# Kernel tuning notes

Hardware: AMD Instinct MI355X
Metric: run time of the kernel (lower is better)

The kernel has to match this reference:

```python
import jax, jax.numpy as jnp
import numpy as np

# ViT-Small config
L, D, H, HD = 12, 384, 6, 64
P, IMG, NCLS = 16, 224, 1000
NPATCH = (IMG // P) ** 2  # 196
GAMMA, MIN_TOKENS, EPS = 0.5, 16, 1e-6
SCALE = HD ** -0.5


def _ln(x, w, b, eps=1e-6):
    mu = jnp.mean(x, axis=-1, keepdims=True)
    var = jnp.var(x, axis=-1, keepdims=True)
    return (x - mu) * jax.lax.rsqrt(var + eps) * w + b


def _qkv_split(xn, w, b):
    # xn: [B, Nt, D] -> q,k,v each [B, H, Nt, HD]
    B, Nt, _ = xn.shape
    qkv = (xn @ w.T + b).reshape(B, Nt, 3, H, HD).transpose(2, 0, 3, 1, 4)
    return qkv[0], qkv[1], qkv[2]


def _vit_forward(x, patch_w, patch_b, cls_token, pos_embed,
                 ln1_w, ln1_b, qkv_w, qkv_b, proj_w, proj_b,
                 ln2_w, ln2_b, fc1_w, fc1_b, fc2_w, fc2_b,
                 norm_w, norm_b, head_w, head_b, keep_schedule=None):
    B = x.shape[0]
    # patch embed: conv stride 16 -> [B, D, 14, 14] -> [B, 196, D]
    xp = jax.lax.conv_general_dilated(x, patch_w, (P, P), 'VALID',
                                      dimension_numbers=('NCHW', 'OIHW', 'NCHW'))
    xp = xp.reshape(B, D, NPATCH).transpose(0, 2, 1) + patch_b
    cls = jnp.broadcast_to(cls_token, (B, 1, D))
    xt = jnp.concatenate([cls, xp], axis=1) + pos_embed  # [B, 197, D]

    N = NPATCH
    prev_mass = jnp.asarray(1.0, jnp.float32)
    schedule = []
    for l in range(L):
        if keep_schedule is not None:
            keep_idx = keep_schedule[l]
        elif N > MIN_TOKENS:
            # CLS-only attention importance scoring (cheap pass)
            xn = _ln(xt, ln1_w[l], ln1_b[l])
            q, k, v = _qkv_split(xn, qkv_w[l], qkv_b[l])
            a_cls = jax.nn.softmax(jnp.einsum('bhqd,bhkd->bhqk', q[:, :, :1], k) * SCALE, axis=-1)[:, :, 0, :]  # [B,H,Nt]
            vnorm = jnp.linalg.norm(v, axis=-1)  # [B,H,Nt]
            imp = (a_cls * vnorm).mean(axis=1)   # [B,Nt]
            imp_p = imp[:, 1:]                   # patch importance
            mass = jnp.mean(imp_p.sum(-1) / (imp.sum(-1) + EPS))
            keep_ratio = float(jnp.clip(GAMMA * mass / (prev_mass + EPS), 0.0, 1.0))
            N_next = max(MIN_TOKENS, int(N * keep_ratio))
            if N_next < N:
                scores = imp_p.mean(0)  # shared keep set across batch (index_select semantics)
                top = jax.lax.top_k(scores, N_next)[1]
                keep_idx = jnp.concatenate([jnp.zeros((1,), jnp.int32),
                                            jnp.sort(top).astype(jnp.int32) + 1])
            else:
                keep_idx = None
            prev_mass = mass
        else:
            keep_idx = None
        schedule.append(keep_idx)
        if keep_idx is not None:
            xt = jnp.take(xt, keep_idx, axis=1)
            N = int(keep_idx.shape[0]) - 1

        # full transformer block on surviving tokens
        Nt = xt.shape[1]
        xn = _ln(xt, ln1_w[l], ln1_b[l])
        q, k, v = _qkv_split(xn, qkv_w[l], qkv_b[l])
        a = jax.nn.softmax(jnp.einsum('bhqd,bhkd->bhqk', q, k) * SCALE, axis=-1)
        o = jnp.einsum('bhqk,bhkd->bhqd', a, v).transpose(0, 2, 1, 3).reshape(B, Nt, D)
        xt = xt + o @ proj_w[l].T + proj_b[l]
        h = _ln(xt, ln2_w[l], ln2_b[l])
        h = jax.nn.gelu(h @ fc1_w[l].T + fc1_b[l], approximate=False)
        xt = xt + h @ fc2_w[l].T + fc2_b[l]

    xt = _ln(xt, norm_w, norm_b)
    logits = xt[:, 0] @ head_w.T + head_b
    return logits, schedule


def setup_inputs() -> dict:
    key = jax.random.key(0)
    ks = jax.random.split(key, 10)
    rn = lambda k, s, sc=0.02: jax.random.normal(k, s, jnp.float32) * sc
    return {
        'x': jax.random.normal(ks[0], (64, 3, IMG, IMG), jnp.float32),
        'patch_w': rn(ks[1], (D, 3, P, P)),
        'patch_b': jnp.zeros((D,), jnp.float32),
        'cls_token': rn(ks[2], (1, 1, D)),
        'pos_embed': rn(ks[3], (1, NPATCH + 1, D)),
        'ln1_w': jnp.ones((L, D), jnp.float32), 'ln1_b': jnp.zeros((L, D), jnp.float32),
        'qkv_w': rn(ks[4], (L, 3 * D, D)), 'qkv_b': jnp.zeros((L, 3 * D), jnp.float32),
        'proj_w': rn(ks[5], (L, D, D)), 'proj_b': jnp.zeros((L, D), jnp.float32),
        'ln2_w': jnp.ones((L, D), jnp.float32), 'ln2_b': jnp.zeros((L, D), jnp.float32),
        'fc1_w': rn(ks[6], (L, 4 * D, D)), 'fc1_b': jnp.zeros((L, 4 * D), jnp.float32),
        'fc2_w': rn(ks[7], (L, D, 4 * D)), 'fc2_b': jnp.zeros((L, D), jnp.float32),
        'norm_w': jnp.ones((D,), jnp.float32), 'norm_b': jnp.zeros((D,), jnp.float32),
        'head_w': rn(ks[8], (NCLS, D)), 'head_b': jnp.zeros((NCLS,), jnp.float32),
    }


def reference(x, patch_w, patch_b, cls_token, pos_embed, ln1_w, ln1_b, qkv_w, qkv_b,
              proj_w, proj_b, ln2_w, ln2_b, fc1_w, fc1_b, fc2_w, fc2_b,
              norm_w, norm_b, head_w, head_b):
    logits, _ = _vit_forward(x, patch_w, patch_b, cls_token, pos_embed, ln1_w, ln1_b,
                             qkv_w, qkv_b, proj_w, proj_b, ln2_w, ln2_b,
                             fc1_w, fc1_b, fc2_w, fc2_b, norm_w, norm_b, head_w, head_b)
    return logits
```

## Files before the change

kernel.cpp:

```cpp
#include <hip/hip_runtime.h>
#include <hip/hip_bf16.h>

static constexpr int kL = 12;
static constexpr int kD = 384;
static constexpr int kH = 6;
static constexpr int kB = 64;
static constexpr int kNP = 196;
static constexpr int kBAND = 197;
static constexpr int kNCLS = 1000;
static constexpr float kSCALE = 0.125f;
static constexpr float kEPS = 1e-6f;
static constexpr size_t kWQ = (size_t)kB * kH * kBAND * 64;

typedef __attribute__((ext_vector_type(8))) short short8;
typedef __attribute__((ext_vector_type(4))) float f32x4;

__device__ __forceinline__ float gelu_f(float x) {
    return 0.5f * x * (1.0f + erff(x * 0.70710678118654752440f));
}
__device__ __forceinline__ unsigned short f2bf(float x) {
    __hip_bfloat16 h = __float2bfloat16(x);
    return *(unsigned short*)&h;
}
__device__ __forceinline__ float bf2f(unsigned short u) {
    __hip_bfloat16 h = *(__hip_bfloat16*)&u;
    return __bfloat162float(h);
}

__global__ __launch_bounds__(384) void k_init(int* si, float* sf,
                                              const float* __restrict__ cls,
                                              const float* __restrict__ pos,
                                              float* __restrict__ xtA,
                                              float2* __restrict__ pstats) {
    int b = blockIdx.x, c = threadIdx.x;
    float v = cls[c] + pos[c];
    xtA[(size_t)b * kBAND * kD + c] = v;
    __shared__ float r1[384], r2[384];
    r1[c] = v; r2[c] = v * v;
    __syncthreads();
    if (c < 128) { r1[c] += r1[c + 128] + r1[c + 256]; r2[c] += r2[c + 128] + r2[c + 256]; }
    __syncthreads();
    for (int st = 64; st; st >>= 1) {
        if (c < st) { r1[c] += r1[c + st]; r2[c] += r2[c + st]; }
        __syncthreads();
    }
    if (c == 0) {
        pstats[(size_t)(b * kBAND) * 8 + 0] = make_float2(r1[0], r2[0]);
#pragma unroll
        for (int nn = 1; nn < 6; ++nn) pstats[(size_t)(b * kBAND) * 8 + nn] = make_float2(0.f, 0.f);
        if (b == 0) { si[0] = kBAND; sf[0] = 1.0f; }
    }
}

__global__ __launch_bounds__(256) void k_cvtall(
    const float* __restrict__ s0, const float* __restrict__ s1, const float* __restrict__ s2,
    const float* __restrict__ s3, const float* __restrict__ s4,
    __hip_bfloat16* __restrict__ d0, __hip_bfloat16* __restrict__ d1, __hip_bfloat16* __restrict__ d2,
    __hip_bfloat16* __restrict__ d3, __hip_bfloat16* __restrict__ d4) {
    const int c0 = 73728, c1 = 1400832, c2 = 1843200, c3 = 3612672, c4 = 5382144;
    int stride = gridDim.x * 256;
    for (int i = blockIdx.x * 256 + threadIdx.x; i < c4; i += stride) {
        const float* src; __hip_bfloat16* dst; int off;
        if (i < c0)      { src = s0; dst = d0; off = i; }
        else if (i < c1) { src = s1; dst = d1; off = i - c0; }
        else if (i < c2) { src = s2; dst = d2; off = i - c1; }
        else if (i < c3) { src = s3; dst = d3; off = i - c2; }
        else             { src = s4; dst = d4; off = i - c3; }
        float4 v = ((const float4*)src)[off];
        dst[4 * off + 0] = __float2bfloat16(v.x);
        dst[4 * off + 1] = __float2bfloat16(v.y);
        dst[4 * off + 2] = __float2bfloat16(v.z);
        dst[4 * off + 3] = __float2bfloat16(v.w);
    }
}

__global__ __launch_bounds__(256) void k_im2col(const float* __restrict__ x, __hip_bfloat16* __restrict__ A) {
    int pt = blockIdx.x;
    int b = pt / kNP, t = pt - b * kNP;
    int py = t / 14, px = t - py * 14;
    const float* xb = x + (size_t)b * 3 * 224 * 224;
    __hip_bfloat16* arow = A + (size_t)pt * 768;
    for (int k = threadIdx.x; k < 768; k += 256) {
        int c = k >> 8;
        int r = k & 255;
        int ky = r >> 4, kx = r & 15;
        arow[k] = __float2bfloat16(xb[((size_t)c * 224 + py * 16 + ky) * 224 + px * 16 + kx]);
    }
}

template<int OUT_BF16, int ACT_GELU, int MODE, int LNA, int STATS>
__global__ __launch_bounds__(256) void k_mgemm(
    const void* __restrict__ Av, int lda,
    const unsigned short* __restrict__ W, int K,
    const float* __restrict__ bias,
    void* __restrict__ Cv, int ldc,
    const float* __restrict__ R,
    const int* __restrict__ keepR,
    const float* __restrict__ lnw, const float* __restrict__ lnb,
    int rT, int nT, int band,
    const int* __restrict__ NtPtr, int ntConst,
    const float2* __restrict__ pstatsIn, float2* __restrict__ pstatsOut)
{
    __shared__ __align__(16) unsigned char pool[18432];
    unsigned short (*As)[72] = (unsigned short (*)[72])pool;
    unsigned short (*Ws)[72] = (unsigned short (*)[72])(pool + 9216);
    float (*Cs)[66] = (float (*)[66])pool;
    unsigned short (*Cu)[76] = (unsigned short (*)[76])pool;
    __shared__ float mus[64], rss[64];

    int Nt = NtPtr ? NtPtr[0] : ntConst;
    unsigned int rowsTotal = (unsigned int)kB * (unsigned int)Nt;

    int L = blockIdx.x;
    int xcd = L & 7;
    int m = L >> 3;
    int n = m % nT;
    int r = (m / nT) * 8 + xcd;
    if (r >= rT) return;
    unsigned int r0 = (unsigned int)r * 64;
    int n0 = n * 64;
    if (r0 >= rowsTotal) return;

    int tid = threadIdx.x;
    int srow = tid >> 3;
    int scol = (tid & 7) << 3;

    unsigned int rv0 = r0 + srow, rv1 = r0 + srow + 32;
    bool v0 = rv0 < rowsTotal, v1 = rv1 < rowsTotal;
    const unsigned short* ah0 = nullptr; const unsigned short* ah1 = nullptr;
    const float* af0 = nullptr; const float* af1 = nullptr;
    if (v0) {
        unsigned int bb = rv0 / (unsigned int)Nt, tt = rv0 - bb * Nt;
        size_t prow = (size_t)bb * band + tt;
        if (LNA) af0 = (const float*)Av + prow * lda;
        else     ah0 = (const unsigned short*)Av + prow * lda;
    }
    if (v1) {
        unsigned int bb = rv1 / (unsigned int)Nt, tt = rv1 - bb * Nt;
        size_t prow = (size_t)bb * band + tt;
        if (LNA) af1 = (const float*)Av + prow * lda;
        else     ah1 = (const unsigned short*)Av + prow * lda;
    }
    const unsigned short* wp0 = W + (size_t)(n0 + srow) * K;
    const unsigned short* wp1 = W + (size_t)(n0 + srow + 32) * K;

    float mu0 = 0.f, rs0 = 0.f, mu1 = 0.f, rs1 = 0.f;
    if (LNA) {
        if (tid < 64) {
            unsigned int rv = r0 + tid;
            float mu = 0.f, rsd = 0.f;
            if (rv < rowsTotal) {
                unsigned int bb = rv / (unsigned int)Nt, tt = rv - bb * Nt;
                const float2* ps = pstatsIn + ((size_t)bb * band + tt) * 8;
                float s1 = 0.f, s2 = 0.f;
#pragma unroll
                for (int nn = 0; nn < 6; ++nn) { float2 p = ps[nn]; s1 += p.x; s2 += p.y; }
                mu = s1 * (1.f / 384.f);
                float var = fmaxf(s2 * (1.f / 384.f) - mu * mu, 0.f);
                rsd = rsqrtf(var + kEPS);
            }
            mus[tid] = mu; rss[tid] = rsd;
        }
        __syncthreads();
        mu0 = mus[srow]; rs0 = rss[srow];
        mu1 = mus[srow + 32]; rs1 = rss[srow + 32];
    }

    int wave = tid >> 6, lane = tid & 63;
    int wr32 = ((wave >> 1) & 1) * 32, wc32 = (wave & 1) * 32;
    int l15 = lane & 15, l4 = lane >> 4;

    f32x4 acc00 = {}, acc01 = {}, acc10 = {}, acc11 = {};

    for (int k0 = 0; k0 < K; k0 += 64) {
        uint4 zero = make_uint4(0, 0, 0, 0);
        uint4 a0 = zero, a1 = zero;
        uint4 w0 = *(const uint4*)(wp0 + k0 + scol);
        uint4 w1 = *(const uint4*)(wp1 + k0 + scol);
        if (LNA) {
            float4 lw0 = *(const float4*)(lnw + k0 + scol);
            float4 lw1 = *(const float4*)(lnw + k0 + scol + 4);
            float4 lb0 = *(const float4*)(lnb + k0 + scol);
            float4 lb1 = *(const float4*)(lnb + k0 + scol + 4);
            if (v0) {
                float4 x0 = *(const float4*)(af0 + k0 + scol);
                float4 x1 = *(const float4*)(af0 + k0 + scol + 4);
                unsigned short p[8];
                p[0] = f2bf((x0.x - mu0) * rs0 * lw0.x + lb0.x);
                p[1] = f2bf((x0.y - mu0) * rs0 * lw0.y + lb0.y);
                p[2] = f2bf((x0.z - mu0) * rs0 * lw0.z + lb0.z);
                p[3] = f2bf((x0.w - mu0) * rs0 * lw0.w + lb0.w);
                p[4] = f2bf((x1.x - mu0) * rs0 * lw1.x + lb1.x);
                p[5] = f2bf((x1.y - mu0) * rs0 * lw1.y + lb1.y);
                p[6] = f2bf((x1.z - mu0) * rs0 * lw1.z + lb1.z);
                p[7] = f2bf((x1.w - mu0) * rs0 * lw1.w + lb1.w);
                a0 = *(uint4*)p;
            }
            if (v1) {
                float4 x0 = *(const float4*)(af1 + k0 + scol);
                float4 x1 = *(const float4*)(af1 + k0 + scol + 4);
                unsigned short p[8];
                p[0] = f2bf((x0.x - mu1) * rs1 * lw0.x + lb0.x);
                p[1] = f2bf((x0.y - mu1) * rs1 * lw0.y + lb0.y);
                p[2] = f2bf((x0.z - mu1) * rs1 * lw0.z + lb0.z);
                p[3] = f2bf((x0.w - mu1) * rs1 * lw0.w + lb0.w);
                p[4] = f2bf((x1.x - mu1) * rs1 * lw1.x + lb1.x);
                p[5] = f2bf((x1.y - mu1) * rs1 * lw1.y + lb1.y);
                p[6] = f2bf((x1.z - mu1) * rs1 * lw1.z + lb1.z);
                p[7] = f2bf((x1.w - mu1) * rs1 * lw1.w + lb1.w);
                a1 = *(uint4*)p;
            }
        } else {
            a0 = v0 ? *(const uint4*)(ah0 + k0 + scol) : zero;
            a1 = v1 ? *(const uint4*)(ah1 + k0 + scol) : zero;
        }
        __syncthreads();
        *(uint4*)&As[srow][scol] = a0;
        *(uint4*)&As[srow + 32][scol] = a1;
        *(uint4*)&Ws[srow][scol] = w0;
        *(uint4*)&Ws[srow + 32][scol] = w1;
        __syncthreads();
#pragma unroll
        for (int ks = 0; ks < 2; ++ks) {
            short8 af_0 = *(const short8*)&As[wr32 + l15][ks * 32 + l4 * 8];
            short8 af_1 = *(const short8*)&As[wr32 + 16 + l15][ks * 32 + l4 * 8];
            short8 bf_0 = *(const short8*)&Ws[wc32 + l15][ks * 32 + l4 * 8];
            short8 bf_1 = *(const short8*)&Ws[wc32 + 16 + l15][ks * 32 + l4 * 8];
            acc00 = __builtin_amdgcn_mfma_f32_16x16x32_bf16(af_0, bf_0, acc00, 0, 0, 0);
            acc01 = __builtin_amdgcn_mfma_f32_16x16x32_bf16(af_0, bf_1, acc01, 0, 0, 0);
            acc10 = __builtin_amdgcn_mfma_f32_16x16x32_bf16(af_1, bf_0, acc10, 0, 0, 0);
            acc11 = __builtin_amdgcn_mfma_f32_16x16x32_bf16(af_1, bf_1, acc11, 0, 0, 0);
        }
    }

    __syncthreads();
    f32x4 accs[2][2] = { { acc00, acc01 }, { acc10, acc11 } };
#pragma unroll
    for (int fi = 0; fi < 2; ++fi) {
        int lrow = wr32 + fi * 16 + l4 * 4;
        unsigned int rvb = r0 + lrow;
#pragma unroll
        for (int fj = 0; fj < 2; ++fj) {
            int lcol = wc32 + fj * 16 + l15;
            float bv = bias ? bias[n0 + lcol] : 0.f;
#pragma unroll
            for (int rr = 0; rr < 4; ++rr) {
                unsigned int rv = rvb + rr;
                float v = accs[fi][fj][rr] + bv;
                if (ACT_GELU) v = gelu_f(v);
                if (MODE == 2) {
                    if (rv < rowsTotal) {
                        unsigned int bb = rv / (unsigned int)Nt;
                        unsigned int tt = rv - bb * (unsigned int)Nt;
                        v += R[(size_t)(tt + 1) * kD + n0 + lcol];
                    }
                } else if (R && rv < rowsTotal) {
                    unsigned int bb = rv / (unsigned int)Nt;
                    unsigned int tt = rv - bb * (unsigned int)Nt;
                    size_t rrow = keepR ? ((size_t)bb * band + keepR[tt]) : ((size_t)bb * band + tt);
                    v += R[rrow * ldc + n0 + lcol];
                }
                if (OUT_BF16) Cu[lrow + rr][lcol] = f2bf(v);
                else          Cs[lrow + rr][lcol] = v;
            }
        }
    }
    __syncthreads();

    if (OUT_BF16) {
#pragma unroll
        for (int i = 0; i < 2; ++i) {
            int id = tid + (i << 8);
            int row = id >> 3, c2 = id & 7;
            unsigned int rv = r0 + row;
            if (rv < rowsTotal) {
                unsigned int bb = rv / (unsigned int)Nt;
                unsigned int tt = rv - bb * (unsigned int)Nt;
                uint4 val = *(const uint4*)&Cu[row][c2 << 3];
                if (MODE == 1) {
                    int which = n0 >= 768 ? 2 : (n0 >= 384 ? 1 : 0);
                    int hh = (n0 - which * 384) >> 6;
                    *(uint4*)((__hip_bfloat16*)Cv + (size_t)which * kWQ +
                              (((size_t)bb * kH + hh) * kBAND + tt) * 64 + (c2 << 3)) = val;
                } else {
                    size_t prow = (size_t)bb * band + tt;
                    *(uint4*)((__hip_bfloat16*)Cv + prow * ldc + n0 + (c2 << 3)) = val;
                }
            }
        }
    } else {
#pragma unroll
        for (int i = 0; i < 4; ++i) {
            int id = tid + (i << 8);
            int row = id >> 4, c4 = id & 15;
            unsigned int rv = r0 + row;
            if (rv < rowsTotal) {
                unsigned int bb = rv / (unsigned int)Nt;
                unsigned int tt = rv - bb * (unsigned int)Nt;
                float4 val = *(const float4*)&Cs[row][c4 << 2];
                if (MODE == 2) {
                    *(float4*)((float*)Cv + ((size_t)bb * kBAND + tt + 1) * ldc + n0 + (c4 << 2)) = val;
                } else {
                    *(float4*)((float*)Cv + ((size_t)bb * band + tt) * ldc + n0 + (c4 << 2)) = val;
                }
                if (STATS) {
                    float s1 = (val.x + val.y) + (val.z + val.w);
                    float s2 = (val.x * val.x + val.y * val.y) + (val.z * val.z + val.w * val.w);
#pragma unroll
                    for (int off = 1; off < 16; off <<= 1) {
                        s1 += __shfl_xor(s1, off, 64);
                        s2 += __shfl_xor(s2, off, 64);
                    }
                    if (c4 == 0) {
                        size_t sridx = (MODE == 2) ? ((size_t)bb * kBAND + tt + 1)
                                                   : ((size_t)bb * band + tt);
                        pstatsOut[sridx * 8 + n] = make_float2(s1, s2);
                    }
                }
            }
        }
    }
}

__global__ __launch_bounds__(256) void k_decA(const __hip_bfloat16* __restrict__ qsplit,
                                              float* __restrict__ imph, float* __restrict__ sabh,
                                              const int* __restrict__ si) {
    int Nt = si[0];
    if (Nt - 1 <= 16) return;
    int tid = threadIdx.x, w = tid >> 6, lane = tid & 63;
    int bh = blockIdx.x;
    __shared__ float qs[64];
    __shared__ float sdot[224], svn[224];
    __shared__ float red[256];
    const __hip_bfloat16* qp = qsplit + (size_t)bh * kBAND * 64;
    const __hip_bfloat16* kp = qsplit + kWQ + (size_t)bh * kBAND * 64;
    const __hip_bfloat16* vp = qsplit + 2 * kWQ + (size_t)bh * kBAND * 64;
    if (tid < 64) qs[tid] = __bfloat162float(qp[tid]);
    __syncthreads();
    float qv = qs[lane];
    for (int j = w; j < Nt; j += 8) {
        int j2 = j + 4;
        bool has2 = j2 < Nt;
        float k1 = __bfloat162float(kp[(size_t)j * 64 + lane]);
        float v1 = __bfloat162float(vp[(size_t)j * 64 + lane]);
        float k2 = has2 ? __bfloat162float(kp[(size_t)j2 * 64 + lane]) : 0.f;
        float v2 = has2 ? __bfloat162float(vp[(size_t)j2 * 64 + lane]) : 0.f;
        float p1 = qv * k1, n1 = v1 * v1;
        float p2 = qv * k2, n2 = v2 * v2;
#pragma unroll
        for (int off = 1; off < 64; off <<= 1) {
            p1 += __shfl_xor(p1, off, 64); n1 += __shfl_xor(n1, off, 64);
            p2 += __shfl_xor(p2, off, 64); n2 += __shfl_xor(n2, off, 64);
        }
        if (lane == 0) {
            sdot[j] = p1 * kSCALE; svn[j] = sqrtf(n1);
            if (has2) { sdot[j2] = p2 * kSCALE; svn[j2] = sqrtf(n2); }
        }
    }
    __syncthreads();
    float s = (tid < Nt) ? sdot[tid] : -INFINITY;
    red[tid] = s; __syncthreads();
    for (int st = 128; st; st >>= 1) { if (tid < st) red[tid] = fmaxf(red[tid], red[tid + st]); __syncthreads(); }
    float mmax = red[0]; __syncthreads();
    float e = (tid < Nt) ? expf(s - mmax) : 0.f;
    red[tid] = e; __syncthreads();
    for (int st = 128; st; st >>= 1) { if (tid < st) red[tid] += red[tid + st]; __syncthreads(); }
    float inv = 1.f / red[0];
    float val = (tid < Nt) ? e * inv * svn[tid] : 0.f;
    if (tid < Nt) imph[(size_t)bh * kBAND + tid] = val;
    __syncthreads();
    red[tid] = val; __syncthreads();
    for (int st = 128; st; st >>= 1) { if (tid < st) red[tid] += red[tid + st]; __syncthreads(); }
    if (tid == 0) { sabh[2 * bh] = red[0]; sabh[2 * bh + 1] = val; }
}

__global__ __launch_bounds__(256) void k_decB(int* __restrict__ si, float* __restrict__ sf,
                                              const float* __restrict__ imph,
                                              const float* __restrict__ sabh,
                                              int* __restrict__ keep) {
    int Nt = si[0];
    int tid = threadIdx.x;
    if (Nt - 1 <= 16) {
        for (int j = tid; j < Nt; j += 256) keep[j] = j;
        return;
    }
    int N = Nt - 1;
    __shared__ float red[256];
    float v = 0.f;
    if (tid < kB) {
        float sa = 0.f, i0 = 0.f;
#pragma unroll
        for (int hh = 0; hh < kH; ++hh) {
            sa += sabh[2 * (tid * kH + hh)];
            i0 += sabh[2 * (tid * kH + hh) + 1];
        }
        sa *= (1.f / 6.f); i0 *= (1.f / 6.f);
        v = (sa - i0) / (sa + kEPS);
    }
    red[tid] = v; __syncthreads();
    for (int st = 128; st; st >>= 1) { if (tid < st) red[tid] += red[tid + st]; __syncthreads(); }
    float mass = red[0] * (1.f / 64.f);
    float prev = sf[0];
    float ratio = 0.5f * mass / (prev + kEPS);
    ratio = fminf(fmaxf(ratio, 0.f), 1.f);
    int N_next = (int)((double)N * (double)ratio);
    if (N_next < 16) N_next = 16;
    if (tid == 0) sf[0] = mass;
    __syncthreads();
    if (N_next >= N) {
        for (int j = tid; j < Nt; j += 256) keep[j] = j;
        return;
    }
    __shared__ float sc[200];
    __shared__ int flag[200];
    if (tid < N) {
        float a0 = 0.f, a1 = 0.f, a2 = 0.f, a3 = 0.f;
        const float* p = imph + tid + 1;
#pragma unroll 4
        for (int q = 0; q < kB * kH; q += 4) {
            a0 += p[(size_t)(q + 0) * kBAND];
            a1 += p[(size_t)(q + 1) * kBAND];
            a2 += p[(size_t)(q + 2) * kBAND];
            a3 += p[(size_t)(q + 3) * kBAND];
        }
        sc[tid] = (a0 + a1) + (a2 + a3);
    }
    __syncthreads();
    if (tid < N) {
        float s2 = sc[tid];
        int rank = 0;
        for (int i = 0; i < N; ++i) {
            float o2 = sc[i];
            rank += (o2 > s2) || (o2 == s2 && i < tid);
        }
        flag[tid] = (rank < N_next) ? 1 : 0;
    }
    __syncthreads();
    if (tid == 0) {
        keep[0] = 0;
        int pos = 1;
        for (int j = 0; j < N; ++j) if (flag[j]) keep[pos++] = j + 1;
        si[0] = N_next + 1;
    }
}

__global__ __launch_bounds__(256) void k_attn2(const __hip_bfloat16* __restrict__ qsplit,
                                               __hip_bfloat16* __restrict__ o,
                                               const int* __restrict__ si,
                                               const int* __restrict__ keep) {
    __shared__ __align__(16) unsigned short Kb[224][72];
    __shared__ __align__(16) unsigned short Vt[64][228];
    __shared__ __align__(16) unsigned short Pb[4][16][228];
    int Nt = si[0];
    int bh = blockIdx.x;
    int b = bh / kH, h = bh - b * kH;
    int tid = threadIdx.x, w = tid >> 6, lane = tid & 63;
    int l15 = lane & 15, l4 = lane >> 4;
    int nJT = (Nt + 15) >> 4;
    int nKT = (Nt + 31) >> 5;
    int NTP = nKT << 5;

    const unsigned short* qb = (const unsigned short*)qsplit + (size_t)bh * kBAND * 64;
    const unsigned short* kb = (const unsigned short*)qsplit + kWQ + (size_t)bh * kBAND * 64;
    const unsigned short* vb = (const unsigned short*)qsplit + 2 * kWQ + (size_t)bh * kBAND * 64;

    {
        int rr = tid >> 3;
        int c8 = (tid & 7) << 3;
        for (int r = rr; r < NTP; r += 32) {
            uint4 kv = make_uint4(0, 0, 0, 0), vv = make_uint4(0, 0, 0, 0);
            if (r < Nt) {
                int old = keep[r];
                kv = *(const uint4*)(kb + ((size_t)old << 6) + c8);
                vv = *(const uint4*)(vb + ((size_t)old << 6) + c8);
            }
            *(uint4*)&Kb[r][c8] = kv;
            const unsigned short* vs = (const unsigned short*)&vv;
#pragma unroll
            for (int e = 0; e < 8; ++e) Vt[c8 + e][r] = vs[e];
        }
    }
    __syncthreads();

    for (int strip = w; strip < nJT; strip += 4) {
        int tq = (strip << 4) + l15;
        int told = (tq < Nt) ? keep[tq] : 0;
        const unsigned short* qrow = qb + ((size_t)told << 6) + (l4 << 3);
        short8 qf0 = *(const short8*)(qrow);
        short8 qf1 = *(const short8*)(qrow + 32);

        f32x4 sv[13];
#pragma unroll
        for (int jt = 0; jt < 13; ++jt) {
            if (jt < nJT) {
                const unsigned short* kr = &Kb[(jt << 4) + l15][l4 << 3];
                short8 kf0 = *(const short8*)(kr);
                short8 kf1 = *(const short8*)(kr + 32);
                f32x4 a = {};
                a = __builtin_amdgcn_mfma_f32_16x16x32_bf16(qf0, kf0, a, 0, 0, 0);
                a = __builtin_amdgcn_mfma_f32_16x16x32_bf16(qf1, kf1, a, 0, 0, 0);
                sv[jt] = a;
            }
        }
        float mx[4] = { -INFINITY, -INFINITY, -INFINITY, -INFINITY };
#pragma unroll
        for (int jt = 0; jt < 13; ++jt) if (jt < nJT) {
            bool ok = ((jt << 4) + l15) < Nt;
#pragma unroll
            for (int r = 0; r < 4; ++r) {
                float s = ok ? sv[jt][r] * kSCALE : -INFINITY;
                sv[jt][r] = s;
                mx[r] = fmaxf(mx[r], s);
            }
        }
#pragma unroll
        for (int r = 0; r < 4; ++r) {
            mx[r] = fmaxf(mx[r], __shfl_xor(mx[r], 1, 64));
            mx[r] = fmaxf(mx[r], __shfl_xor(mx[r], 2, 64));
            mx[r] = fmaxf(mx[r], __shfl_xor(mx[r], 4, 64));
            mx[r] = fmaxf(mx[r], __shfl_xor(mx[r], 8, 64));
        }
        float sm[4] = { 0.f, 0.f, 0.f, 0.f };
#pragma unroll
        for (int jt = 0; jt < 13; ++jt) if (jt < nJT) {
#pragma unroll
            for (int r = 0; r < 4; ++r) {
                float p = expf(sv[jt][r] - mx[r]);
                sv[jt][r] = p;
                sm[r] += p;
            }
        }
#pragma unroll
        for (int r = 0; r < 4; ++r) {
            sm[r] += __shfl_xor(sm[r], 1, 64);
            sm[r] += __shfl_xor(sm[r], 2, 64);
            sm[r] += __shfl_xor(sm[r], 4, 64);
            sm[r] += __shfl_xor(sm[r], 8, 64);
            sm[r] = 1.f / sm[r];
        }
#pragma unroll
        for (int jt = 0; jt < 13; ++jt) if (jt < nJT) {
#pragma unroll
            for (int r = 0; r < 4; ++r)
                Pb[w][(l4 << 2) + r][(jt << 4) + l15] = f2bf(sv[jt][r] * sm[r]);
        }
        for (int c = (nJT << 4) + lane; c < NTP; c += 64) {
#pragma unroll
            for (int rr2 = 0; rr2 < 16; ++rr2) Pb[w][rr2][c] = 0;
        }
        asm volatile("s_waitcnt lgkmcnt(0)" ::: "memory");
        __builtin_amdgcn_sched_barrier(0);

        f32x4 oacc[4] = { {}, {}, {}, {} };
#pragma unroll
        for (int kt = 0; kt < 7; ++kt) if (kt < nKT) {
            short8 pf = *(const short8*)&Pb[w][l15][(kt << 5) + (l4 << 3)];
#pragma unroll
            for (int dt = 0; dt < 4; ++dt) {
                short8 vf = *(const short8*)&Vt[(dt << 4) + l15][(kt << 5) + (l4 << 3)];
                oacc[dt] = __builtin_amdgcn_mfma_f32_16x16x32_bf16(pf, vf, oacc[dt], 0, 0, 0);
            }
        }
#pragma unroll
        for (int dt = 0; dt < 4; ++dt) {
#pragma unroll
            for (int r = 0; r < 4; ++r) {
                int tqo = (strip << 4) + (l4 << 2) + r;
                if (tqo < Nt)
                    o[((size_t)b * kBAND + tqo) * kD + h * 64 + (dt << 4) + l15] =
                        __float2bfloat16(oacc[dt][r]);
            }
        }
    }
}

__global__ __launch_bounds__(256) void k_head(const float* __restrict__ X,
                                              const float* __restrict__ nw, const float* __restrict__ nb,
                                              const float* __restrict__ hw, const float* __restrict__ hb,
                                              float* __restrict__ out) {
    int b = blockIdx.x >> 2;
    int tid = threadIdx.x;
    __shared__ float xs[384];
    __shared__ float red[256];
    const float* row = X + (size_t)b * kBAND * kD;
    float s1 = 0.f, s2 = 0.f;
    for (int c = tid; c < 384; c += 256) { float v = row[c]; xs[c] = v; s1 += v; s2 += v * v; }
    red[tid] = s1; __syncthreads();
    for (int st = 128; st; st >>= 1) { if (tid < st) red[tid] += red[tid + st]; __syncthreads(); }
    float sum = red[0]; __syncthreads();
    red[tid] = s2; __syncthreads();
    for (int st = 128; st; st >>= 1) { if (tid < st) red[tid] += red[tid + st]; __syncthreads(); }
    float sq = red[0];
    float mu = sum * (1.f / 384.f);
    float var = fmaxf(sq * (1.f / 384.f) - mu * mu, 0.f);
    float rs = rsqrtf(var + kEPS);
    __syncthreads();
    for (int c = tid; c < 384; c += 256) xs[c] = (xs[c] - mu) * rs * nw[c] + nb[c];
    __syncthreads();
    int n = ((blockIdx.x & 3) << 8) + tid;
    if (n >= kNCLS) return;
    const float* wrow = hw + (size_t)n * kD;
    float acc = 0.f;
#pragma unroll 8
    for (int d = 0; d < kD; d += 4) {
        float4 w4 = *(const float4*)(wrow + d);
        acc += xs[d] * w4.x + xs[d + 1] * w4.y + xs[d + 2] * w4.z + xs[d + 3] * w4.w;
    }
    out[(size_t)b * kNCLS + n] = acc + hb[n];
}

extern "C" void kernel_launch(void* const* d_in, const int* in_sizes, int n_in,
                              void* d_out, int out_size, void* d_ws, size_t ws_size,
                              hipStream_t stream) {
    const float* x       = (const float*)d_in[0];
    const float* patch_w = (const float*)d_in[1];
    const float* patch_b = (const float*)d_in[2];
    const float* cls_tok = (const float*)d_in[3];
    const float* pos     = (const float*)d_in[4];
    const float* ln1w    = (const float*)d_in[5];
    const float* ln1b    = (const float*)d_in[6];
    const float* qkvw    = (const float*)d_in[7];
    const float* qkvb    = (const float*)d_in[8];
    const float* projw   = (const float*)d_in[9];
    const float* projb   = (const float*)d_in[10];
    const float* ln2w    = (const float*)d_in[11];
    const float* ln2b    = (const float*)d_in[12];
    const float* fc1w    = (const float*)d_in[13];
    const float* fc1b    = (const float*)d_in[14];
    const float* fc2w    = (const float*)d_in[15];
    const float* fc2b    = (const float*)d_in[16];
    const float* normw   = (const float*)d_in[17];
    const float* normb   = (const float*)d_in[18];
    const float* headw   = (const float*)d_in[19];
    const float* headb   = (const float*)d_in[20];
    float* out = (float*)d_out;

    char* ws = (char*)d_ws;
    const size_t MB = 1024ull * 1024ull;
    int*   si   = (int*)ws;
    float* sf   = (float*)(ws + 64);
    int*   keep = (int*)(ws + 256);
    float* sabh = (float*)(ws + 4096);
    float* imph = (float*)(ws + 16384);
    float* xtA  = (float*)(ws + 1 * MB);
    float* xtB  = (float*)(ws + 21 * MB);
    __hip_bfloat16* obuf = (__hip_bfloat16*)(ws + 41 * MB);
    __hip_bfloat16* Aim    = (__hip_bfloat16*)(ws + 51 * MB);
    __hip_bfloat16* qsplit = (__hip_bfloat16*)(ws + 51 * MB);
    __hip_bfloat16* hbuf   = (__hip_bfloat16*)(ws + 51 * MB);
    __hip_bfloat16* wpat = (__hip_bfloat16*)(ws + 110 * MB);
    __hip_bfloat16* wqkv = (__hip_bfloat16*)(ws + 111 * MB);
    __hip_bfloat16* wprj = (__hip_bfloat16*)(ws + 122 * MB);
    __hip_bfloat16* wfc1 = (__hip_bfloat16*)(ws + 126 * MB);
    __hip_bfloat16* wfc2 = (__hip_bfloat16*)(ws + 141 * MB);
    float2* pstats = (float2*)(ws + 156 * MB);

    k_init<<<64, 384, 0, stream>>>(si, sf, cls_tok, pos, xtA, pstats);
    k_cvtall<<<2048, 256, 0, stream>>>(patch_w, qkvw, projw, fc1w, fc2w,
                                       wpat, wqkv, wprj, wfc1, wfc2);

    k_im2col<<<kB * kNP, 256, 0, stream>>>(x, Aim);
    k_mgemm<0, 0, 2, 0, 1><<<8 * 6 * 25, 256, 0, stream>>>(
        (const void*)Aim, 768, (const unsigned short*)wpat, 768,
        patch_b, xtA, kD, pos, (const int*)nullptr,
        (const float*)nullptr, (const float*)nullptr,
        196, 6, 196, (const int*)nullptr, 196,
        (const float2*)nullptr, pstats);

    float* cur = xtA; float* oth = xtB;
    for (int l = 0; l < kL; ++l) {
        const float* l1w = ln1w + l * kD;  const float* l1b = ln1b + l * kD;
        const __hip_bfloat16* qw = wqkv + (size_t)l * 1152 * kD;
        const float* qb = qkvb + l * 1152;
        const __hip_bfloat16* pw = wprj + (size_t)l * kD * kD;
        const float* pb = projb + l * kD;
        const float* l2w = ln2w + l * kD;  const float* l2b = ln2b + l * kD;
        const __hip_bfloat16* f1w = wfc1 + (size_t)l * 1536 * kD;
        const float* f1b = fc1b + l * 1536;
        const __hip_bfloat16* f2w = wfc2 + (size_t)l * kD * 1536;
        const float* f2b = fc2b + l * kD;

        k_mgemm<1, 0, 1, 1, 0><<<8 * 18 * 25, 256, 0, stream>>>(
            (const void*)cur, kD, (const unsigned short*)qw, kD,
            qb, qsplit, 1152, (const float*)nullptr, (const int*)nullptr,
            l1w, l1b, 197, 18, kBAND, si, 0,
            (const float2*)pstats, (float2*)nullptr);
        k_decA<<<kB * kH, 256, 0, stream>>>(qsplit, imph, sabh, si);
        k_decB<<<1, 256, 0, stream>>>(si, sf, imph, sabh, keep);
        k_attn2<<<kB * kH, 256, 0, stream>>>(qsplit, obuf, si, keep);
        k_mgemm<0, 0, 0, 0, 1><<<8 * 6 * 25, 256, 0, stream>>>(
            (const void*)obuf, kD, (const unsigned short*)pw, kD,
            pb, oth, kD, cur, keep,
            (const float*)nullptr, (const float*)nullptr,
            197, 6, kBAND, si, 0,
            (const float2*)nullptr, pstats);
        { float* tmp = cur; cur = oth; oth = tmp; }
        k_mgemm<1, 1, 0, 1, 0><<<8 * 24 * 25, 256, 0, stream>>>(
            (const void*)cur, kD, (const unsigned short*)f1w, kD,
            f1b, hbuf, 1536, (const float*)nullptr, (const int*)nullptr,
            l2w, l2b, 197, 24, kBAND, si, 0,
            (const float2*)pstats, (float2*)nullptr);
        k_mgemm<0, 0, 0, 0, 1><<<8 * 6 * 25, 256, 0, stream>>>(
            (const void*)hbuf, 1536, (const unsigned short*)f2w, 1536,
            f2b, cur, kD, cur, (const int*)nullptr,
            (const float*)nullptr, (const float*)nullptr,
            197, 6, kBAND, si, 0,
            (const float2*)nullptr, pstats);
    }

    k_head<<<kB * 4, 256, 0, stream>>>(cur, normw, normb, headw, headb, out);
}
```

Before: 1.251 ms.

## Widen GEMM tiles to 64x128 and transpose importance buffer for coalesced reduction

The generic MFMA GEMM now computes a 64x128 output tile per block: each wave holds 2x4 accumulators, more weight rows are staged in LDS, and fp32 output is written in two 64-column halves. This halves the number of blocks, so each A tile is loaded and LayerNorm-normalized half as often. Per-head stats are written per 64-column half, so the stats layout stays the same. Separately, the importance buffer is stored token-major so the single-block decision kernel can reduce it with coalesced float4 loads across more threads. The larger tile uses more LDS and registers, which lowers occupancy, and with fewer blocks the grid may underfill the GPU for small token counts.

```diff
diff --git a/kernel.cpp b/kernel.cpp
--- a/kernel.cpp
+++ b/kernel.cpp
@@ -11,6 +11,7 @@
 static constexpr float kSCALE = 0.125f;
 static constexpr float kEPS = 1e-6f;
 static constexpr size_t kWQ = (size_t)kB * kH * kBAND * 64;
+static constexpr int kBH = kB * kH;
 
 typedef __attribute__((ext_vector_type(8))) short short8;
 typedef __attribute__((ext_vector_type(4))) float f32x4;
@@ -21,10 +22,6 @@
 __device__ __forceinline__ unsigned short f2bf(float x) {
     __hip_bfloat16 h = __float2bfloat16(x);
     return *(unsigned short*)&h;
-}
-__device__ __forceinline__ float bf2f(unsigned short u) {
-    __hip_bfloat16 h = *(__hip_bfloat16*)&u;
-    return __bfloat162float(h);
 }
 
 __global__ __launch_bounds__(384) void k_init(int* si, float* sf,
@@ -101,11 +98,11 @@
     const int* __restrict__ NtPtr, int ntConst,
     const float2* __restrict__ pstatsIn, float2* __restrict__ pstatsOut)
 {
-    __shared__ __align__(16) unsigned char pool[18432];
+    __shared__ __align__(16) unsigned char pool[27648];
     unsigned short (*As)[72] = (unsigned short (*)[72])pool;
     unsigned short (*Ws)[72] = (unsigned short (*)[72])(pool + 9216);
-    float (*Cs)[66] = (float (*)[66])pool;
-    unsigned short (*Cu)[76] = (unsigned short (*)[76])pool;
+    float (*Cs)[68] = (float (*)[68])pool;
+    unsigned short (*Cu)[136] = (unsigned short (*)[136])pool;
     __shared__ float mus[64], rss[64];
 
     int Nt = NtPtr ? NtPtr[0] : ntConst;
@@ -118,7 +115,7 @@
     int r = (m / nT) * 8 + xcd;
     if (r >= rT) return;
     unsigned int r0 = (unsigned int)r * 64;
-    int n0 = n * 64;
+    int n0 = n * 128;
     if (r0 >= rowsTotal) return;
 
     int tid = threadIdx.x;
@@ -143,6 +140,8 @@
     }
     const unsigned short* wp0 = W + (size_t)(n0 + srow) * K;
     const unsigned short* wp1 = W + (size_t)(n0 + srow + 32) * K;
+    const unsigned short* wp2 = W + (size_t)(n0 + srow + 64) * K;
+    const unsigned short* wp3 = W + (size_t)(n0 + srow + 96) * K;
 
     float mu0 = 0.f, rs0 = 0.f, mu1 = 0.f, rs1 = 0.f;
     if (LNA) {
@@ -167,16 +166,23 @@
     }
 
     int wave = tid >> 6, lane = tid & 63;
-    int wr32 = ((wave >> 1) & 1) * 32, wc32 = (wave & 1) * 32;
+    int wr32 = ((wave >> 1) & 1) << 5;
+    int wc64 = (wave & 1) << 6;
     int l15 = lane & 15, l4 = lane >> 4;
 
-    f32x4 acc00 = {}, acc01 = {}, acc10 = {}, acc11 = {};
+    f32x4 acc[2][4];
+#pragma unroll
+    for (int i = 0; i < 2; ++i)
+#pragma unroll
+        for (int j = 0; j < 4; ++j) acc[i][j] = (f32x4){};
 
     for (int k0 = 0; k0 < K; k0 += 64) {
         uint4 zero = make_uint4(0, 0, 0, 0);
         uint4 a0 = zero, a1 = zero;
         uint4 w0 = *(const uint4*)(wp0 + k0 + scol);
         uint4 w1 = *(const uint4*)(wp1 + k0 + scol);
+        uint4 w2 = *(const uint4*)(wp2 + k0 + scol);
+        uint4 w3 = *(const uint4*)(wp3 + k0 + scol);
         if (LNA) {
             float4 lw0 = *(const float4*)(lnw + k0 + scol);
             float4 lw1 = *(const float4*)(lnw + k0 + scol + 4);
@@ -219,69 +225,59 @@
         *(uint4*)&As[srow + 32][scol] = a1;
         *(uint4*)&Ws[srow][scol] = w0;
         *(uint4*)&Ws[srow + 32][scol] = w1;
+        *(uint4*)&Ws[srow + 64][scol] = w2;
+        *(uint4*)&Ws[srow + 96][scol] = w3;
         __syncthreads();
 #pragma unroll
         for (int ks = 0; ks < 2; ++ks) {
-            short8 af_0 = *(const short8*)&As[wr32 + l15][ks * 32 + l4 * 8];
-            short8 af_1 = *(const short8*)&As[wr32 + 16 + l15][ks * 32 + l4 * 8];
-            short8 bf_0 = *(const short8*)&Ws[wc32 + l15][ks * 32 + l4 * 8];
-            short8 bf_1 = *(const short8*)&Ws[wc32 + 16 + l15][ks * 32 + l4 * 8];
-            acc00 = __builtin_amdgcn_mfma_f32_16x16x32_bf16(af_0, bf_0, acc00, 0, 0, 0);
-            acc01 = __builtin_amdgcn_mfma_f32_16x16x32_bf16(af_0, bf_1, acc01, 0, 0, 0);
-            acc10 = __builtin_amdgcn_mfma_f32_16x16x32_bf16(af_1, bf_0, acc10, 0, 0, 0);
-            acc11 = __builtin_amdgcn_mfma_f32_16x16x32_bf16(af_1, bf_1, acc11, 0, 0, 0);
-        }
-    }
-
-    __syncthreads();
-    f32x4 accs[2][2] = { { acc00, acc01 }, { acc10, acc11 } };
-#pragma unroll
-    for (int fi = 0; fi < 2; ++fi) {
-        int lrow = wr32 + fi * 16 + l4 * 4;
-        unsigned int rvb = r0 + lrow;
-#pragma unroll
-        for (int fj = 0; fj < 2; ++fj) {
-            int lcol = wc32 + fj * 16 + l15;
-            float bv = bias ? bias[n0 + lcol] : 0.f;
-#pragma unroll
-            for (int rr = 0; rr < 4; ++rr) {
-                unsigned int rv = rvb + rr;
-                float v = accs[fi][fj][rr] + bv;
-                if (ACT_GELU) v = gelu_f(v);
-                if (MODE == 2) {
-                    if (rv < rowsTotal) {
-                        unsigned int bb = rv / (unsigned int)Nt;
-                        unsigned int tt = rv - bb * (unsigned int)Nt;
-                        v += R[(size_t)(tt + 1) * kD + n0 + lcol];
-                    }
-                } else if (R && rv < rowsTotal) {
-                    unsigned int bb = rv / (unsigned int)Nt;
-                    unsigned int tt = rv - bb * (unsigned int)Nt;
-                    size_t rrow = keepR ? ((size_t)bb * band + keepR[tt]) : ((size_t)bb * band + tt);
-                    v += R[rrow * ldc + n0 + lcol];
+            short8 af_0 = *(const short8*)&As[wr32 + l15][(ks << 5) + (l4 << 3)];
+            short8 af_1 = *(const short8*)&As[wr32 + 16 + l15][(ks << 5) + (l4 << 3)];
+            short8 bfr[4];
+#pragma unroll
+            for (int j = 0; j < 4; ++j)
+                bfr[j] = *(const short8*)&Ws[wc64 + (j << 4) + l15][(ks << 5) + (l4 << 3)];
+#pragma unroll
+            for (int j = 0; j < 4; ++j) {
+                acc[0][j] = __builtin_amdgcn_mfma_f32_16x16x32_bf16(af_0, bfr[j], acc[0][j], 0, 0, 0);
+                acc[1][j] = __builtin_amdgcn_mfma_f32_16x16x32_bf16(af_1, bfr[j], acc[1][j], 0, 0, 0);
+            }
+        }
+    }
+
+    __syncthreads();
+
+    if (OUT_BF16) {
+#pragma unroll
+        for (int i = 0; i < 2; ++i) {
+            int lrow = wr32 + (i << 4) + (l4 << 2);
+#pragma unroll
+            for (int j = 0; j < 4; ++j) {
+                int lcol = wc64 + (j << 4) + l15;
+                float bv = bias ? bias[n0 + lcol] : 0.f;
+#pragma unroll
+                for (int rr = 0; rr < 4; ++rr) {
+                    float v = acc[i][j][rr] + bv;
+                    if (ACT_GELU) v = gelu_f(v);
+                    Cu[lrow + rr][lcol] = f2bf(v);
                 }
-                if (OUT_BF16) Cu[lrow + rr][lcol] = f2bf(v);
-                else          Cs[lrow + rr][lcol] = v;
-            }
-        }
-    }
-    __syncthreads();
-
-    if (OUT_BF16) {
-#pragma unroll
-        for (int i = 0; i < 2; ++i) {
-            int id = tid + (i << 8);
-            int row = id >> 3, c2 = id & 7;
+            }
+        }
+        __syncthreads();
+#pragma unroll
+        for (int i2 = 0; i2 < 4; ++i2) {
+            int id = tid + (i2 << 8);
+            int row = id >> 4, c2 = id & 15;
             unsigned int rv = r0 + row;
             if (rv < rowsTotal) {
                 unsigned int bb = rv / (unsigned int)Nt;
                 unsigned int tt = rv - bb * (unsigned int)Nt;
                 uint4 val = *(const uint4*)&Cu[row][c2 << 3];
                 if (MODE == 1) {
-                    int which = n0 >= 768 ? 2 : (n0 >= 384 ? 1 : 0);
-                    int hh = (n0 - which * 384) >> 6;
+                    int gc = n0 + (c2 << 3);
+                    int which = gc >= 768 ? 2 : (gc >= 384 ? 1 : 0);
+                    int hh = (gc - which * 384) >> 6;
                     *(uint4*)((__hip_bfloat16*)Cv + (size_t)which * kWQ +
-                              (((size_t)bb * kH + hh) * kBAND + tt) * 64 + (c2 << 3)) = val;
+                              (((size_t)bb * kH + hh) * kBAND + tt) * 64 + (gc & 63)) = val;
                 } else {
                     size_t prow = (size_t)bb * band + tt;
                     *(uint4*)((__hip_bfloat16*)Cv + prow * ldc + n0 + (c2 << 3)) = val;
@@ -290,34 +286,72 @@
         }
     } else {
 #pragma unroll
-        for (int i = 0; i < 4; ++i) {
-            int id = tid + (i << 8);
-            int row = id >> 4, c4 = id & 15;
-            unsigned int rv = r0 + row;
-            if (rv < rowsTotal) {
-                unsigned int bb = rv / (unsigned int)Nt;
-                unsigned int tt = rv - bb * (unsigned int)Nt;
-                float4 val = *(const float4*)&Cs[row][c4 << 2];
-                if (MODE == 2) {
-                    *(float4*)((float*)Cv + ((size_t)bb * kBAND + tt + 1) * ldc + n0 + (c4 << 2)) = val;
-                } else {
-                    *(float4*)((float*)Cv + ((size_t)bb * band + tt) * ldc + n0 + (c4 << 2)) = val;
-                }
-                if (STATS) {
-                    float s1 = (val.x + val.y) + (val.z + val.w);
-                    float s2 = (val.x * val.x + val.y * val.y) + (val.z * val.z + val.w * val.w);
-#pragma unroll
-                    for (int off = 1; off < 16; off <<= 1) {
-                        s1 += __shfl_xor(s1, off, 64);
-                        s2 += __shfl_xor(s2, off, 64);
-                    }
-                    if (c4 == 0) {
-                        size_t sridx = (MODE == 2) ? ((size_t)bb * kBAND + tt + 1)
-                                                   : ((size_t)bb * band + tt);
-                        pstatsOut[sridx * 8 + n] = make_float2(s1, s2);
+        for (int half = 0; half < 2; ++half) {
+            if ((wave & 1) == half) {
+#pragma unroll
+                for (int i = 0; i < 2; ++i) {
+                    int lrow = wr32 + (i << 4) + (l4 << 2);
+                    unsigned int rvb = r0 + lrow;
+#pragma unroll
+                    for (int j = 0; j < 4; ++j) {
+                        int lcl = (j << 4) + l15;
+                        int gcol = n0 + (half << 6) + lcl;
+                        float bv = bias ? bias[gcol] : 0.f;
+#pragma unroll
+                        for (int rr = 0; rr < 4; ++rr) {
+                            unsigned int rv = rvb + rr;
+                            float v = acc[i][j][rr] + bv;
+                            if (ACT_GELU) v = gelu_f(v);
+                            if (MODE == 2) {
+                                if (rv < rowsTotal) {
+                                    unsigned int bb = rv / (unsigned int)Nt;
+                                    unsigned int tt = rv - bb * (unsigned int)Nt;
+                                    v += R[(size_t)(tt + 1) * kD + gcol];
+                                }
+                            } else if (R && rv < rowsTotal) {
+                                unsigned int bb = rv / (unsigned int)Nt;
+                                unsigned int tt = rv - bb * (unsigned int)Nt;
+                                size_t rrow = keepR ? ((size_t)bb * band + keepR[tt]) : ((size_t)bb * band + tt);
+                                v += R[rrow * ldc + gcol];
+                            }
+                            Cs[lrow + rr][lcl] = v;
+                        }
                     }
                 }
             }
+            __syncthreads();
+#pragma unroll
+            for (int i2 = 0; i2 < 4; ++i2) {
+                int id = tid + (i2 << 8);
+                int row = id >> 4, c4 = id & 15;
+                unsigned int rv = r0 + row;
+                if (rv < rowsTotal) {
+                    unsigned int bb = rv / (unsigned int)Nt;
+                    unsigned int tt = rv - bb * (unsigned int)Nt;
+                    float4 val = *(const float4*)&Cs[row][c4 << 2];
+                    int gbase = n0 + (half << 6) + (c4 << 2);
+                    if (MODE == 2) {
+                        *(float4*)((float*)Cv + ((size_t)bb * kBAND + tt + 1) * ldc + gbase) = val;
+                    } else {
+                        *(float4*)((float*)Cv + ((size_t)bb * band + tt) * ldc + gbase) = val;
+                    }
+                    if (STATS) {
+                        float s1 = (val.x + val.y) + (val.z + val.w);
+                        float s2 = (val.x * val.x + val.y * val.y) + (val.z * val.z + val.w * val.w);
+#pragma unroll
+                        for (int off = 1; off < 16; off <<= 1) {
+                            s1 += __shfl_xor(s1, off, 64);
+                            s2 += __shfl_xor(s2, off, 64);
+                        }
+                        if (c4 == 0) {
+                            size_t sridx = (MODE == 2) ? ((size_t)bb * kBAND + tt + 1)
+                                                       : ((size_t)bb * band + tt);
+                            pstatsOut[sridx * 8 + (n << 1) + half] = make_float2(s1, s2);
+                        }
+                    }
+                }
+            }
+            __syncthreads();
         }
     }
 }
@@ -367,7 +401,7 @@
     for (int st = 128; st; st >>= 1) { if (tid < st) red[tid] += red[tid + st]; __syncthreads(); }
     float inv = 1.f / red[0];
     float val = (tid < Nt) ? e * inv * svn[tid] : 0.f;
-    if (tid < Nt) imph[(size_t)bh * kBAND + tid] = val;
+    if (tid < Nt) imph[(size_t)tid * kBH + bh] = val;
     __syncthreads();
     red[tid] = val; __syncthreads();
     for (int st = 128; st; st >>= 1) { if (tid < st) red[tid] += red[tid + st]; __syncthreads(); }
@@ -411,20 +445,25 @@
         for (int j = tid; j < Nt; j += 256) keep[j] = j;
         return;
     }
+    __shared__ float scq[200][4];
     __shared__ float sc[200];
     __shared__ int flag[200];
-    if (tid < N) {
+    for (int task = tid; task < N * 4; task += 256) {
+        int row = task >> 2, seg = task & 3;
+        const float4* p = (const float4*)(imph + (size_t)(row + 1) * kBH) + seg * 24;
         float a0 = 0.f, a1 = 0.f, a2 = 0.f, a3 = 0.f;
-        const float* p = imph + tid + 1;
-#pragma unroll 4
-        for (int q = 0; q < kB * kH; q += 4) {
-            a0 += p[(size_t)(q + 0) * kBAND];
-            a1 += p[(size_t)(q + 1) * kBAND];
-            a2 += p[(size_t)(q + 2) * kBAND];
-            a3 += p[(size_t)(q + 3) * kBAND];
-        }
-        sc[tid] = (a0 + a1) + (a2 + a3);
-    }
+#pragma unroll
+        for (int q = 0; q < 24; q += 4) {
+            float4 x0 = p[q + 0], x1 = p[q + 1], x2 = p[q + 2], x3 = p[q + 3];
+            a0 += (x0.x + x0.y) + (x0.z + x0.w);
+            a1 += (x1.x + x1.y) + (x1.z + x1.w);
+            a2 += (x2.x + x2.y) + (x2.z + x2.w);
+            a3 += (x3.x + x3.y) + (x3.z + x3.w);
+        }
+        scq[row][seg] = (a0 + a1) + (a2 + a3);
+    }
+    __syncthreads();
+    if (tid < N) sc[tid] = (scq[tid][0] + scq[tid][1]) + (scq[tid][2] + scq[tid][3]);
     __syncthreads();
     if (tid < N) {
         float s2 = sc[tid];
@@ -660,11 +699,11 @@
                                        wpat, wqkv, wprj, wfc1, wfc2);
 
     k_im2col<<<kB * kNP, 256, 0, stream>>>(x, Aim);
-    k_mgemm<0, 0, 2, 0, 1><<<8 * 6 * 25, 256, 0, stream>>>(
+    k_mgemm<0, 0, 2, 0, 1><<<8 * 3 * 25, 256, 0, stream>>>(
         (const void*)Aim, 768, (const unsigned short*)wpat, 768,
         patch_b, xtA, kD, pos, (const int*)nullptr,
         (const float*)nullptr, (const float*)nullptr,
-        196, 6, 196, (const int*)nullptr, 196,
+        196, 3, 196, (const int*)nullptr, 196,
         (const float2*)nullptr, pstats);
 
     float* cur = xtA; float* oth = xtB;
@@ -680,31 +719,31 @@
         const __hip_bfloat16* f2w = wfc2 + (size_t)l * kD * 1536;
         const float* f2b = fc2b + l * kD;
 
-        k_mgemm<1, 0, 1, 1, 0><<<8 * 18 * 25, 256, 0, stream>>>(
+        k_mgemm<1, 0, 1, 1, 0><<<8 * 9 * 25, 256, 0, stream>>>(
             (const void*)cur, kD, (const unsigned short*)qw, kD,
             qb, qsplit, 1152, (const float*)nullptr, (const int*)nullptr,
-            l1w, l1b, 197, 18, kBAND, si, 0,
+            l1w, l1b, 197, 9, kBAND, si, 0,
             (const float2*)pstats, (float2*)nullptr);
         k_decA<<<kB * kH, 256, 0, stream>>>(qsplit, imph, sabh, si);
         k_decB<<<1, 256, 0, stream>>>(si, sf, imph, sabh, keep);
         k_attn2<<<kB * kH, 256, 0, stream>>>(qsplit, obuf, si, keep);
-        k_mgemm<0, 0, 0, 0, 1><<<8 * 6 * 25, 256, 0, stream>>>(
+        k_mgemm<0, 0, 0, 0, 1><<<8 * 3 * 25, 256, 0, stream>>>(
             (const void*)obuf, kD, (const unsigned short*)pw, kD,
             pb, oth, kD, cur, keep,
             (const float*)nullptr, (const float*)nullptr,
-            197, 6, kBAND, si, 0,
+            197, 3, kBAND, si, 0,
             (const float2*)nullptr, pstats);
         { float* tmp = cur; cur = oth; oth = tmp; }
-        k_mgemm<1, 1, 0, 1, 0><<<8 * 24 * 25, 256, 0, stream>>>(
+        k_mgemm<1, 1, 0, 1, 0><<<8 * 12 * 25, 256, 0, stream>>>(
             (const void*)cur, kD, (const unsigned short*)f1w, kD,
             f1b, hbuf, 1536, (const float*)nullptr, (const int*)nullptr,
-            l2w, l2b, 197, 24, kBAND, si, 0,
+            l2w, l2b, 197, 12, kBAND, si, 0,
             (const float2*)pstats, (float2*)nullptr);
-        k_mgemm<0, 0, 0, 0, 1><<<8 * 6 * 25, 256, 0, stream>>>(
+        k_mgemm<0, 0, 0, 0, 1><<<8 * 3 * 25, 256, 0, stream>>>(
             (const void*)hbuf, 1536, (const unsigned short*)f2w, 1536,
             f2b, cur, kD, cur, (const int*)nullptr,
             (const float*)nullptr, (const float*)nullptr,
-            197, 6, kBAND, si, 0,
+            197, 3, kBAND, si, 0,
             (const float2*)nullptr, pstats);
     }
 
```

Measured after the change: 1.643 ms. +31.3%, slower.

## Fuse im2col into patch-embed GEMM and transpose importance buffer for coalesced reduction

Applied to the files above, without the earlier changes.

Removes the separate im2col kernel: the patch-embed GEMM (MODE 2) now reads fp32 image pixels directly, computing the patch offsets in its load path and converting to bf16. This avoids writing and rereading the intermediate bf16 im2col matrix. The per-head importance buffer is stored token-major so the keep-set scoring kernel can sum it with float4 loads split across four threads per token. The commit also changes the column offset in the qkv split store, which looks like a fix for tiles narrower than 64.

```diff
diff --git a/kernel.cpp b/kernel.cpp
--- a/kernel.cpp
+++ b/kernel.cpp
@@ -11,6 +11,7 @@
 static constexpr float kSCALE = 0.125f;
 static constexpr float kEPS = 1e-6f;
 static constexpr size_t kWQ = (size_t)kB * kH * kBAND * 64;
+static constexpr int kBH = kB * kH;
 
 typedef __attribute__((ext_vector_type(8))) short short8;
 typedef __attribute__((ext_vector_type(4))) float f32x4;
@@ -21,10 +22,6 @@
 __device__ __forceinline__ unsigned short f2bf(float x) {
     __hip_bfloat16 h = __float2bfloat16(x);
     return *(unsigned short*)&h;
-}
-__device__ __forceinline__ float bf2f(unsigned short u) {
-    __hip_bfloat16 h = *(__hip_bfloat16*)&u;
-    return __bfloat162float(h);
 }
 
 __global__ __launch_bounds__(384) void k_init(int* si, float* sf,
@@ -74,20 +71,6 @@
     }
 }
 
-__global__ __launch_bounds__(256) void k_im2col(const float* __restrict__ x, __hip_bfloat16* __restrict__ A) {
-    int pt = blockIdx.x;
-    int b = pt / kNP, t = pt - b * kNP;
-    int py = t / 14, px = t - py * 14;
-    const float* xb = x + (size_t)b * 3 * 224 * 224;
-    __hip_bfloat16* arow = A + (size_t)pt * 768;
-    for (int k = threadIdx.x; k < 768; k += 256) {
-        int c = k >> 8;
-        int r = k & 255;
-        int ky = r >> 4, kx = r & 15;
-        arow[k] = __float2bfloat16(xb[((size_t)c * 224 + py * 16 + ky) * 224 + px * 16 + kx]);
-    }
-}
-
 template<int OUT_BF16, int ACT_GELU, int MODE, int LNA, int STATS>
 __global__ __launch_bounds__(256) void k_mgemm(
     const void* __restrict__ Av, int lda,
@@ -129,17 +112,31 @@
     bool v0 = rv0 < rowsTotal, v1 = rv1 < rowsTotal;
     const unsigned short* ah0 = nullptr; const unsigned short* ah1 = nullptr;
     const float* af0 = nullptr; const float* af1 = nullptr;
-    if (v0) {
-        unsigned int bb = rv0 / (unsigned int)Nt, tt = rv0 - bb * Nt;
-        size_t prow = (size_t)bb * band + tt;
-        if (LNA) af0 = (const float*)Av + prow * lda;
-        else     ah0 = (const unsigned short*)Av + prow * lda;
-    }
-    if (v1) {
-        unsigned int bb = rv1 / (unsigned int)Nt, tt = rv1 - bb * Nt;
-        size_t prow = (size_t)bb * band + tt;
-        if (LNA) af1 = (const float*)Av + prow * lda;
-        else     ah1 = (const unsigned short*)Av + prow * lda;
+    const float* xb0 = nullptr; const float* xb1 = nullptr;
+    if (MODE == 2) {
+        if (v0) {
+            unsigned int bb = rv0 / (unsigned int)Nt, tt = rv0 - bb * Nt;
+            int py = tt / 14, px = tt - py * 14;
+            xb0 = (const float*)Av + (size_t)bb * 3 * 224 * 224 + (py * 16) * 224 + px * 16;
+        }
+        if (v1) {
+            unsigned int bb = rv1 / (unsigned int)Nt, tt = rv1 - bb * Nt;
+            int py = tt / 14, px = tt - py * 14;
+            xb1 = (const float*)Av + (size_t)bb * 3 * 224 * 224 + (py * 16) * 224 + px * 16;
+        }
+    } else {
+        if (v0) {
+            unsigned int bb = rv0 / (unsigned int)Nt, tt = rv0 - bb * Nt;
+            size_t prow = (size_t)bb * band + tt;
+            if (LNA) af0 = (const float*)Av + prow * lda;
+            else     ah0 = (const unsigned short*)Av + prow * lda;
+        }
+        if (v1) {
+            unsigned int bb = rv1 / (unsigned int)Nt, tt = rv1 - bb * Nt;
+            size_t prow = (size_t)bb * band + tt;
+            if (LNA) af1 = (const float*)Av + prow * lda;
+            else     ah1 = (const unsigned short*)Av + prow * lda;
+        }
     }
     const unsigned short* wp0 = W + (size_t)(n0 + srow) * K;
     const unsigned short* wp1 = W + (size_t)(n0 + srow + 32) * K;
@@ -177,7 +174,29 @@
         uint4 a0 = zero, a1 = zero;
         uint4 w0 = *(const uint4*)(wp0 + k0 + scol);
         uint4 w1 = *(const uint4*)(wp1 + k0 + scol);
-        if (LNA) {
+        if (MODE == 2) {
+            int k = k0 + scol;
+            int c = k >> 8;
+            int rr_ = k & 255;
+            int ky = rr_ >> 4, kx = rr_ & 15;
+            size_t off = (size_t)c * 50176 + (size_t)ky * 224 + kx;
+            if (v0) {
+                float4 x0 = *(const float4*)(xb0 + off);
+                float4 x1 = *(const float4*)(xb0 + off + 4);
+                unsigned short p[8];
+                p[0] = f2bf(x0.x); p[1] = f2bf(x0.y); p[2] = f2bf(x0.z); p[3] = f2bf(x0.w);
+                p[4] = f2bf(x1.x); p[5] = f2bf(x1.y); p[6] = f2bf(x1.z); p[7] = f2bf(x1.w);
+                a0 = *(uint4*)p;
+            }
+            if (v1) {
+                float4 x0 = *(const float4*)(xb1 + off);
+                float4 x1 = *(const float4*)(xb1 + off + 4);
+                unsigned short p[8];
+                p[0] = f2bf(x0.x); p[1] = f2bf(x0.y); p[2] = f2bf(x0.z); p[3] = f2bf(x0.w);
+                p[4] = f2bf(x1.x); p[5] = f2bf(x1.y); p[6] = f2bf(x1.z); p[7] = f2bf(x1.w);
+                a1 = *(uint4*)p;
+            }
+        } else if (LNA) {
             float4 lw0 = *(const float4*)(lnw + k0 + scol);
             float4 lw1 = *(const float4*)(lnw + k0 + scol + 4);
             float4 lb0 = *(const float4*)(lnb + k0 + scol);
@@ -281,7 +300,7 @@
                     int which = n0 >= 768 ? 2 : (n0 >= 384 ? 1 : 0);
                     int hh = (n0 - which * 384) >> 6;
                     *(uint4*)((__hip_bfloat16*)Cv + (size_t)which * kWQ +
-                              (((size_t)bb * kH + hh) * kBAND + tt) * 64 + (c2 << 3)) = val;
+                              (((size_t)bb * kH + hh) * kBAND + tt) * 64 + ((n0 & 63) + (c2 << 3))) = val;
                 } else {
                     size_t prow = (size_t)bb * band + tt;
                     *(uint4*)((__hip_bfloat16*)Cv + prow * ldc + n0 + (c2 << 3)) = val;
@@ -367,7 +386,7 @@
     for (int st = 128; st; st >>= 1) { if (tid < st) red[tid] += red[tid + st]; __syncthreads(); }
     float inv = 1.f / red[0];
     float val = (tid < Nt) ? e * inv * svn[tid] : 0.f;
-    if (tid < Nt) imph[(size_t)bh * kBAND + tid] = val;
+    if (tid < Nt) imph[(size_t)tid * kBH + bh] = val;
     __syncthreads();
     red[tid] = val; __syncthreads();
     for (int st = 128; st; st >>= 1) { if (tid < st) red[tid] += red[tid + st]; __syncthreads(); }
@@ -411,20 +430,25 @@
         for (int j = tid; j < Nt; j += 256) keep[j] = j;
         return;
     }
+    __shared__ float scq[200][4];
     __shared__ float sc[200];
     __shared__ int flag[200];
-    if (tid < N) {
+    for (int task = tid; task < N * 4; task += 256) {
+        int row = task >> 2, seg = task & 3;
+        const float4* p = (const float4*)(imph + (size_t)(row + 1) * kBH) + seg * 24;
         float a0 = 0.f, a1 = 0.f, a2 = 0.f, a3 = 0.f;
-        const float* p = imph + tid + 1;
-#pragma unroll 4
-        for (int q = 0; q < kB * kH; q += 4) {
-            a0 += p[(size_t)(q + 0) * kBAND];
-            a1 += p[(size_t)(q + 1) * kBAND];
-            a2 += p[(size_t)(q + 2) * kBAND];
-            a3 += p[(size_t)(q + 3) * kBAND];
-        }
-        sc[tid] = (a0 + a1) + (a2 + a3);
-    }
+#pragma unroll
+        for (int q = 0; q < 24; q += 4) {
+            float4 x0 = p[q + 0], x1 = p[q + 1], x2 = p[q + 2], x3 = p[q + 3];
+            a0 += (x0.x + x0.y) + (x0.z + x0.w);
+            a1 += (x1.x + x1.y) + (x1.z + x1.w);
+            a2 += (x2.x + x2.y) + (x2.z + x2.w);
+            a3 += (x3.x + x3.y) + (x3.z + x3.w);
+        }
+        scq[row][seg] = (a0 + a1) + (a2 + a3);
+    }
+    __syncthreads();
+    if (tid < N) sc[tid] = (scq[tid][0] + scq[tid][1]) + (scq[tid][2] + scq[tid][3]);
     __syncthreads();
     if (tid < N) {
         float s2 = sc[tid];
@@ -645,7 +669,6 @@
     float* xtA  = (float*)(ws + 1 * MB);
     float* xtB  = (float*)(ws + 21 * MB);
     __hip_bfloat16* obuf = (__hip_bfloat16*)(ws + 41 * MB);
-    __hip_bfloat16* Aim    = (__hip_bfloat16*)(ws + 51 * MB);
     __hip_bfloat16* qsplit = (__hip_bfloat16*)(ws + 51 * MB);
     __hip_bfloat16* hbuf   = (__hip_bfloat16*)(ws + 51 * MB);
     __hip_bfloat16* wpat = (__hip_bfloat16*)(ws + 110 * MB);
@@ -659,9 +682,8 @@
     k_cvtall<<<2048, 256, 0, stream>>>(patch_w, qkvw, projw, fc1w, fc2w,
                                        wpat, wqkv, wprj, wfc1, wfc2);
 
-    k_im2col<<<kB * kNP, 256, 0, stream>>>(x, Aim);
     k_mgemm<0, 0, 2, 0, 1><<<8 * 6 * 25, 256, 0, stream>>>(
-        (const void*)Aim, 768, (const unsigned short*)wpat, 768,
+        (const void*)x, 768, (const unsigned short*)wpat, 768,
         patch_b, xtA, kD, pos, (const int*)nullptr,
         (const float*)nullptr, (const float*)nullptr,
         196, 6, 196, (const int*)nullptr, 196,
```

Result: faster. 1.220 ms (-2.5%).
